# Kernel tuning notes

Hardware: AMD Instinct MI355X
Metric: run time of the kernel (lower is better)

Reference implementation:

```python
import jax, jax.numpy as jnp
import numpy as np

N_NODES = 100000
N_EDGES = 1600000
IN_CH, HID_CH, OUT_CH = 128, 128, 64


def setup_inputs() -> dict:
    key = jax.random.key(0)
    ks = jax.random.split(key, 9)
    x = jax.random.normal(ks[0], (N_NODES, IN_CH), dtype=jnp.float32)
    edge_index = jax.random.randint(ks[1], (2, N_EDGES), 0, N_NODES, dtype=jnp.int64)
    def glorot(k, shape):
        fan_in = shape[1]
        return jax.random.normal(k, shape, dtype=jnp.float32) / jnp.sqrt(jnp.float32(fan_in))
    return {
        "x": x,
        "edge_index": edge_index,
        "W1_l": glorot(ks[2], (HID_CH, IN_CH)),
        "W1_r": glorot(ks[3], (HID_CH, IN_CH)),
        "b1": jnp.zeros((HID_CH,), jnp.float32),
        "W2_l": glorot(ks[4], (HID_CH, HID_CH)),
        "W2_r": glorot(ks[5], (HID_CH, HID_CH)),
        "b2": jnp.zeros((HID_CH,), jnp.float32),
        "W3_l": glorot(ks[6], (OUT_CH, HID_CH)),
        "W3_r": glorot(ks[7], (OUT_CH, HID_CH)),
        "b3": jnp.zeros((OUT_CH,), jnp.float32),
    }


def _sage_conv(x, src, dst, W_l, W_r, b):
    # PyG SAGEConv (aggr='mean', root_weight=True): out = lin_l(mean_j x_j) + lin_r(x_i)
    n = x.shape[0]
    msg = x[src]                                            # [E, C] gather at source
    agg = jax.ops.segment_sum(msg, dst, num_segments=n)     # [N, C] scatter-sum at dest
    cnt = jax.ops.segment_sum(jnp.ones((src.shape[0],), x.dtype), dst, num_segments=n)
    mean = agg / jnp.maximum(cnt, 1.0)[:, None]             # zero-in-degree nodes -> 0
    return mean @ W_l.T + x @ W_r.T + b


def reference(x, edge_index, W1_l, W1_r, b1, W2_l, W2_r, b2, W3_l, W3_r, b3):
    src, dst = edge_index[0], edge_index[1]
    h = jax.nn.relu(_sage_conv(x, src, dst, W1_l, W1_r, b1))
    # F.dropout with training=False is identity (eval mode)
    h = jax.nn.relu(_sage_conv(h, src, dst, W2_l, W2_r, b2))
    return _sage_conv(h, src, dst, W3_l, W3_r, b3)
```

## Files before the change

### kernel.cpp

```cpp
#include <hip/hip_runtime.h>
#include <hip/hip_bf16.h>
#include <cstddef>
#include <cstdint>

#define NBLK(n, b) (((n) + (b) - 1) / (b))

typedef __attribute__((ext_vector_type(8))) short short8;
typedef __attribute__((ext_vector_type(4))) float f32x4;

__device__ inline unsigned short f2bf(float f) {
  union { float f; unsigned u; } v; v.f = f;
  unsigned u = v.u;
  u += 0x7FFFu + ((u >> 16) & 1u);
  return (unsigned short)(u >> 16);
}
__device__ inline float bflo(unsigned u) { union { unsigned u; float f; } v; v.u = u << 16; return v.f; }
__device__ inline float bfhi(unsigned u) { union { unsigned u; float f; } v; v.u = u & 0xFFFF0000u; return v.f; }


__global__ void k_detect(const unsigned* __restrict__ edges, int* __restrict__ flag) {
  if (threadIdx.x == 0 && blockIdx.x == 0) {
    int is64 = 1;
#pragma unroll
    for (int i = 0; i < 16; ++i)
      if (edges[2 * i + 1] != 0u) is64 = 0;
    *flag = is64;
  }
}

__global__ void k_zero_int(int* __restrict__ p, int n) {
  int i = blockIdx.x * blockDim.x + threadIdx.x;
  if (i < n) p[i] = 0;
}

__global__ void k_cast(const float* __restrict__ x, unsigned* __restrict__ xb, int total2) {
  int i = blockIdx.x * blockDim.x + threadIdx.x;
  if (i >= total2) return;
  float2 v = *(const float2*)(x + (size_t)i * 2);
  xb[i] = (unsigned)f2bf(v.x) | ((unsigned)f2bf(v.y) << 16);
}

__global__ void k_prep_w(const float* __restrict__ Wl, const float* __restrict__ Wr,
                         unsigned short* __restrict__ Wb, int total) {
  int i = blockIdx.x * blockDim.x + threadIdx.x;
  if (i >= total) return;
  int nrow = i >> 8, k = i & 255;
  float v = (k < 128) ? Wr[nrow * 128 + k] : Wl[nrow * 128 + (k - 128)];
  Wb[i] = f2bf(v);
}

__global__ void k_hist_rank(const void* __restrict__ edges, const int* __restrict__ flag,
                            int* __restrict__ deg, int* __restrict__ rank, int E) {
  int e = blockIdx.x * blockDim.x + threadIdx.x;
  if (e >= E) return;
  int d;
  if (*flag) d = (int)((const long long*)edges)[(size_t)E + e];
  else       d = ((const int*)edges)[(size_t)E + e];
  rank[e] = atomicAdd(&deg[d], 1);
}

__global__ void k_scan1(const int* __restrict__ deg, int* __restrict__ rowptr,
                        int* __restrict__ partials, int n) {
  __shared__ int sd[256];
  int t = threadIdx.x;
  int base = blockIdx.x * 1024 + t * 4;
  int v[4];
  int sum = 0;
#pragma unroll
  for (int i = 0; i < 4; ++i) {
    int idx = base + i;
    v[i] = (idx < n) ? deg[idx] : 0;
    sum += v[i];
  }
  sd[t] = sum;
  __syncthreads();
  for (int off = 1; off < 256; off <<= 1) {
    int xv = (t >= off) ? sd[t - off] : 0;
    __syncthreads();
    sd[t] += xv;
    __syncthreads();
  }
  int run = sd[t] - sum;
#pragma unroll
  for (int i = 0; i < 4; ++i) {
    int idx = base + i;
    if (idx < n) rowptr[idx] = run;
    run += v[i];
  }
  if (t == 0) partials[blockIdx.x] = sd[255];
}

__global__ void k_scan2(int* __restrict__ partials, int nb) {
  __shared__ int sd[256];
  int t = threadIdx.x;
  int v = (t < nb) ? partials[t] : 0;
  sd[t] = v;
  __syncthreads();
  for (int off = 1; off < 256; off <<= 1) {
    int xv = (t >= off) ? sd[t - off] : 0;
    __syncthreads();
    sd[t] += xv;
    __syncthreads();
  }
  if (t < nb) partials[t] = sd[t] - v;
}

__global__ void k_scan_add(int* __restrict__ rowptr, const int* __restrict__ partials, int n, int E) {
  int i = blockIdx.x * blockDim.x + threadIdx.x;
  if (i < n) rowptr[i] += partials[i >> 10];
  if (blockIdx.x == 0 && threadIdx.x == 0) rowptr[n] = E;
}

__global__ void k_fill2(const void* __restrict__ edges, const int* __restrict__ flag,
                        const int* __restrict__ rowptr, const int* __restrict__ rank,
                        int* __restrict__ srcSorted, int E) {
  int e = blockIdx.x * blockDim.x + threadIdx.x;
  if (e >= E) return;
  int s, d;
  if (*flag) {
    const long long* p = (const long long*)edges;
    s = (int)p[e];
    d = (int)p[(size_t)E + e];
  } else {
    const int* p = (const int*)edges;
    s = p[e];
    d = p[(size_t)E + e];
  }
  srcSorted[rowptr[d] + rank[e]] = s;
}

__global__ void k_aggregate(const unsigned* __restrict__ in, const int* __restrict__ rowptr,
                            const int* __restrict__ srcs, unsigned* __restrict__ mean, int n) {
  int lane = threadIdx.x & 63;
  int w = threadIdx.x >> 6;
  int node = blockIdx.x * 4 + w;
  if (node >= n) return;
  int r0 = rowptr[node], r1 = rowptr[node + 1];
  int sub = lane & 15;
  int eg = lane >> 4;
  float acc[8];
#pragma unroll
  for (int k = 0; k < 8; ++k) acc[k] = 0.f;

  for (int base = r0; base < r1; base += 64) {
    int e = base + lane;
    int sv = (e < r1) ? srcs[e] : 0;
    int cnt = min(64, r1 - base);
    int j = 0;
    for (; j + 8 <= cnt; j += 8) {
      int s0 = __shfl(sv, j + eg);
      int s1 = __shfl(sv, j + 4 + eg);
      uint4 u0 = *(const uint4*)(in + (size_t)s0 * 64 + sub * 4);
      uint4 u1 = *(const uint4*)(in + (size_t)s1 * 64 + sub * 4);
      acc[0] += bflo(u0.x); acc[1] += bfhi(u0.x);
      acc[2] += bflo(u0.y); acc[3] += bfhi(u0.y);
      acc[4] += bflo(u0.z); acc[5] += bfhi(u0.z);
      acc[6] += bflo(u0.w); acc[7] += bfhi(u0.w);
      acc[0] += bflo(u1.x); acc[1] += bfhi(u1.x);
      acc[2] += bflo(u1.y); acc[3] += bfhi(u1.y);
      acc[4] += bflo(u1.z); acc[5] += bfhi(u1.z);
      acc[6] += bflo(u1.w); acc[7] += bfhi(u1.w);
    }
    for (; j < cnt; j += 4) {
      int jj = j + eg;
      int s = __shfl(sv, jj);
      if (jj < cnt) {
        uint4 u = *(const uint4*)(in + (size_t)s * 64 + sub * 4);
        acc[0] += bflo(u.x); acc[1] += bfhi(u.x);
        acc[2] += bflo(u.y); acc[3] += bfhi(u.y);
        acc[4] += bflo(u.z); acc[5] += bfhi(u.z);
        acc[6] += bflo(u.w); acc[7] += bfhi(u.w);
      }
    }
  }

#pragma unroll
  for (int k = 0; k < 8; ++k) {
    acc[k] += __shfl_down(acc[k], 32);
    acc[k] += __shfl_down(acc[k], 16);
  }
  if (eg == 0) {
    float sc = 1.0f / (float)max(r1 - r0, 1);
    uint4 o;
    o.x = (unsigned)f2bf(acc[0] * sc) | ((unsigned)f2bf(acc[1] * sc) << 16);
    o.y = (unsigned)f2bf(acc[2] * sc) | ((unsigned)f2bf(acc[3] * sc) << 16);
    o.z = (unsigned)f2bf(acc[4] * sc) | ((unsigned)f2bf(acc[5] * sc) << 16);
    o.w = (unsigned)f2bf(acc[6] * sc) | ((unsigned)f2bf(acc[7] * sc) << 16);
    *(uint4*)(mean + (size_t)node * 64 + sub * 4) = o;
  }
}

template <int H, bool RELU, bool BF16OUT>
__global__ __launch_bounds__(256) void k_gemm(
    const unsigned short* __restrict__ selfB, const unsigned short* __restrict__ meanB,
    const unsigned short* __restrict__ Wb, const float* __restrict__ bias,
    void* __restrict__ outp, int n) {
  constexpr int TN = H / 32;
  int lane = threadIdx.x & 63;
  int w = threadIdx.x >> 6;
  int wr = w & 1, wc = w >> 1;
  int nodeBase = blockIdx.x * 128 + wr * 64;
  int colBase = wc * (H / 2);
  int l15 = lane & 15, quad = lane >> 4;

  f32x4 acc[4][TN];
#pragma unroll
  for (int t = 0; t < 4; ++t)
#pragma unroll
    for (int j = 0; j < TN; ++j) acc[t][j] = (f32x4){0.f, 0.f, 0.f, 0.f};

#pragma unroll
  for (int c = 0; c < 8; ++c) {
    const unsigned short* A = (c < 4) ? selfB : meanB;
    int ko = (c & 3) * 32 + quad * 8;
    short8 af[4], bfr[TN];
#pragma unroll
    for (int t = 0; t < 4; ++t) {
      int row = nodeBase + t * 16 + l15;
      row = min(row, n - 1);
      af[t] = *(const short8*)(A + (size_t)row * 128 + ko);
    }
#pragma unroll
    for (int j = 0; j < TN; ++j) {
      int cn = colBase + j * 16 + l15;
      bfr[j] = *(const short8*)(Wb + (size_t)cn * 256 + c * 32 + quad * 8);
    }
#pragma unroll
    for (int t = 0; t < 4; ++t)
#pragma unroll
      for (int j = 0; j < TN; ++j)
        acc[t][j] = __builtin_amdgcn_mfma_f32_16x16x32_bf16(af[t], bfr[j], acc[t][j], 0, 0, 0);
  }

#pragma unroll
  for (int j = 0; j < TN; ++j) {
    int col = colBase + j * 16 + l15;
    float bv = bias[col];
#pragma unroll
    for (int t = 0; t < 4; ++t) {
#pragma unroll
      for (int r = 0; r < 4; ++r) {
        int row = nodeBase + t * 16 + quad * 4 + r;
        if (row < n) {
          float v = acc[t][j][r] + bv;
          if (RELU) v = fmaxf(v, 0.f);
          if (BF16OUT) ((unsigned short*)outp)[(size_t)row * H + col] = f2bf(v);
          else ((float*)outp)[(size_t)row * H + col] = v;
        }
      }
    }
  }
}


extern "C" void kernel_launch(void* const* d_in, const int* in_sizes, int n_in,
                              void* d_out, int out_size, void* d_ws, size_t ws_size,
                              hipStream_t stream) {
  (void)n_in; (void)out_size; (void)ws_size;
  const float* x = (const float*)d_in[0];
  const void* edges = d_in[1];
  const float* W1l = (const float*)d_in[2];
  const float* W1r = (const float*)d_in[3];
  const float* b1 = (const float*)d_in[4];
  const float* W2l = (const float*)d_in[5];
  const float* W2r = (const float*)d_in[6];
  const float* b2 = (const float*)d_in[7];
  const float* W3l = (const float*)d_in[8];
  const float* W3r = (const float*)d_in[9];
  const float* b3 = (const float*)d_in[10];
  float* out = (float*)d_out;

  const int N = in_sizes[0] / 128;
  const int E = in_sizes[1] / 2;

  char* ws = (char*)d_ws;
  size_t off = 0;
  auto alloc = [&](size_t bytes) -> char* {
    char* p = ws + off;
    off = (off + bytes + 255) & ~(size_t)255;
    return p;
  };
  int* flag = (int*)alloc(4);
  int* deg = (int*)alloc((size_t)N * 4);
  int* rowptr = (int*)alloc((size_t)(N + 1) * 4);
  int* rank = (int*)alloc((size_t)E * 4);
  int* partials = (int*)alloc(4096);
  int* srcSorted = (int*)alloc((size_t)E * 4);
  unsigned short* xb = (unsigned short*)alloc((size_t)N * 128 * 2);
  unsigned short* mean = (unsigned short*)alloc((size_t)N * 128 * 2);
  unsigned short* h1 = (unsigned short*)alloc((size_t)N * 128 * 2);
  unsigned short* h2 = (unsigned short*)alloc((size_t)N * 128 * 2);
  unsigned short* Wb1 = (unsigned short*)alloc(128 * 256 * 2);
  unsigned short* Wb2 = (unsigned short*)alloc(128 * 256 * 2);
  unsigned short* Wb3 = (unsigned short*)alloc(64 * 256 * 2);

  int nb1 = (N + 1023) / 1024;

  k_detect<<<1, 64, 0, stream>>>((const unsigned*)edges, flag);
  k_zero_int<<<NBLK(N, 256), 256, 0, stream>>>(deg, N);
  k_cast<<<NBLK(N * 64, 256), 256, 0, stream>>>(x, (unsigned*)xb, N * 64);
  k_prep_w<<<NBLK(128 * 256, 256), 256, 0, stream>>>(W1l, W1r, Wb1, 128 * 256);
  k_prep_w<<<NBLK(128 * 256, 256), 256, 0, stream>>>(W2l, W2r, Wb2, 128 * 256);
  k_prep_w<<<NBLK(64 * 256, 256), 256, 0, stream>>>(W3l, W3r, Wb3, 64 * 256);
  k_hist_rank<<<NBLK(E, 256), 256, 0, stream>>>(edges, flag, deg, rank, E);
  k_scan1<<<nb1, 256, 0, stream>>>(deg, rowptr, partials, N);
  k_scan2<<<1, 256, 0, stream>>>(partials, nb1);
  k_scan_add<<<NBLK(N, 256), 256, 0, stream>>>(rowptr, partials, N, E);
  k_fill2<<<NBLK(E, 256), 256, 0, stream>>>(edges, flag, rowptr, rank, srcSorted, E);

  int gAgg = NBLK(N, 4);
  int gGemm = NBLK(N, 128);

  k_aggregate<<<gAgg, 256, 0, stream>>>((const unsigned*)xb, rowptr, srcSorted, (unsigned*)mean, N);
  k_gemm<128, true, true><<<gGemm, 256, 0, stream>>>(xb, mean, Wb1, b1, h1, N);
  k_aggregate<<<gAgg, 256, 0, stream>>>((const unsigned*)h1, rowptr, srcSorted, (unsigned*)mean, N);
  k_gemm<128, true, true><<<gGemm, 256, 0, stream>>>(h1, mean, Wb2, b2, h2, N);
  k_aggregate<<<gAgg, 256, 0, stream>>>((const unsigned*)h2, rowptr, srcSorted, (unsigned*)mean, N);
  k_gemm<64, false, false><<<gGemm, 256, 0, stream>>>(h2, mean, Wb3, b3, out, N);
}
```

Baseline: 522.5 us.

## Replace global-atomic CSR build with two-level bucketed counting sort

Builds the CSR through a bucketed counting sort instead of a per-edge global atomic histogram and scattered fill. Edges are first bucketed by destination block of 512 nodes using shared-memory histograms. Each bucket is then sorted locally in shared memory to produce rowptr and srcSorted. The cast, weight prep, zeroing and format detection kernels are merged into one setup launch to cut launch count. This removes heavily contended global atomics and random scatters, but packs the source and local destination into 32 bits, which assumes node ids below 2^17.

```diff
diff --git a/kernel.cpp b/kernel.cpp
--- a/kernel.cpp
+++ b/kernel.cpp
@@ -17,59 +17,89 @@
 __device__ inline float bflo(unsigned u) { union { unsigned u; float f; } v; v.u = u << 16; return v.f; }
 __device__ inline float bfhi(unsigned u) { union { unsigned u; float f; } v; v.u = u & 0xFFFF0000u; return v.f; }
 
-
-__global__ void k_detect(const unsigned* __restrict__ edges, int* __restrict__ flag) {
-  if (threadIdx.x == 0 && blockIdx.x == 0) {
-    int is64 = 1;
-#pragma unroll
-    for (int i = 0; i < 16; ++i)
-      if (edges[2 * i + 1] != 0u) is64 = 0;
-    *flag = is64;
-  }
-}
-
-__global__ void k_zero_int(int* __restrict__ p, int n) {
-  int i = blockIdx.x * blockDim.x + threadIdx.x;
-  if (i < n) p[i] = 0;
-}
-
-__global__ void k_cast(const float* __restrict__ x, unsigned* __restrict__ xb, int total2) {
-  int i = blockIdx.x * blockDim.x + threadIdx.x;
-  if (i >= total2) return;
-  float2 v = *(const float2*)(x + (size_t)i * 2);
-  xb[i] = (unsigned)f2bf(v.x) | ((unsigned)f2bf(v.y) << 16);
-}
-
-__global__ void k_prep_w(const float* __restrict__ Wl, const float* __restrict__ Wr,
-                         unsigned short* __restrict__ Wb, int total) {
-  int i = blockIdx.x * blockDim.x + threadIdx.x;
-  if (i >= total) return;
+#define BSHIFT 9
+#define BSIZE 512
+
+
+__device__ inline void prep_w_dev(const float* __restrict__ Wl, const float* __restrict__ Wr,
+                                  unsigned short* __restrict__ Wb, int b) {
+  int i = b * 256 + threadIdx.x;
   int nrow = i >> 8, k = i & 255;
   float v = (k < 128) ? Wr[nrow * 128 + k] : Wl[nrow * 128 + (k - 128)];
   Wb[i] = f2bf(v);
 }
 
-__global__ void k_hist_rank(const void* __restrict__ edges, const int* __restrict__ flag,
-                            int* __restrict__ deg, int* __restrict__ rank, int E) {
-  int e = blockIdx.x * blockDim.x + threadIdx.x;
-  if (e >= E) return;
-  int d;
-  if (*flag) d = (int)((const long long*)edges)[(size_t)E + e];
-  else       d = ((const int*)edges)[(size_t)E + e];
-  rank[e] = atomicAdd(&deg[d], 1);
-}
-
-__global__ void k_scan1(const int* __restrict__ deg, int* __restrict__ rowptr,
-                        int* __restrict__ partials, int n) {
+__global__ void k_setup(const float* __restrict__ x, unsigned* __restrict__ xb, int N,
+                        int* __restrict__ bucketCnt, int NB,
+                        const float* __restrict__ W1l, const float* __restrict__ W1r, unsigned short* __restrict__ Wb1,
+                        const float* __restrict__ W2l, const float* __restrict__ W2r, unsigned short* __restrict__ Wb2,
+                        const float* __restrict__ W3l, const float* __restrict__ W3r, unsigned short* __restrict__ Wb3,
+                        const unsigned* __restrict__ edges, int* __restrict__ flag) {
+  int b = blockIdx.x;
+  int gCast = (N * 64 + 255) >> 8;
+  if (b < gCast) {
+    int i = b * 256 + threadIdx.x;
+    if (i < N * 64) {
+      float2 v = *(const float2*)(x + (size_t)i * 2);
+      xb[i] = (unsigned)f2bf(v.x) | ((unsigned)f2bf(v.y) << 16);
+    }
+    return;
+  }
+  b -= gCast;
+  if (b < 128) { prep_w_dev(W1l, W1r, Wb1, b); return; }
+  b -= 128;
+  if (b < 128) { prep_w_dev(W2l, W2r, Wb2, b); return; }
+  b -= 128;
+  if (b < 64) { prep_w_dev(W3l, W3r, Wb3, b); return; }
+  b -= 64;
+  if (b == 0) {
+    for (int i = threadIdx.x; i < NB; i += 256) bucketCnt[i] = 0;
+    if (threadIdx.x == 0) {
+      int is64 = 1;
+#pragma unroll
+      for (int i = 0; i < 16; ++i)
+        if (edges[2 * i + 1] != 0u) is64 = 0;
+      *flag = is64;
+    }
+  }
+}
+
+
+__global__ __launch_bounds__(256) void k_bhist(const void* __restrict__ edges, const int* __restrict__ flag,
+                                               int* __restrict__ bucketCnt, int E, int NB) {
+  __shared__ int h[1024];
+  for (int i = threadIdx.x; i < NB; i += 256) h[i] = 0;
+  __syncthreads();
+  int base_e = blockIdx.x * 4096;
+  bool is64 = (*flag) != 0;
+#pragma unroll
+  for (int k = 0; k < 16; ++k) {
+    int e = base_e + k * 256 + threadIdx.x;
+    if (e < E) {
+      int d;
+      if (is64) d = (int)((const long long*)edges)[(size_t)E + e];
+      else      d = ((const int*)edges)[(size_t)E + e];
+      atomicAdd(&h[d >> BSHIFT], 1);
+    }
+  }
+  __syncthreads();
+  for (int i = threadIdx.x; i < NB; i += 256) {
+    int c = h[i];
+    if (c) atomicAdd(&bucketCnt[i], c);
+  }
+}
+
+__global__ void k_bscan(const int* __restrict__ bucketCnt, int* __restrict__ bucketBase,
+                        int* __restrict__ bucketCursor, int NB, int E) {
   __shared__ int sd[256];
   int t = threadIdx.x;
-  int base = blockIdx.x * 1024 + t * 4;
+  int base = t * 4;
   int v[4];
   int sum = 0;
 #pragma unroll
   for (int i = 0; i < 4; ++i) {
     int idx = base + i;
-    v[i] = (idx < n) ? deg[idx] : 0;
+    v[i] = (idx < NB) ? bucketCnt[idx] : 0;
     sum += v[i];
   }
   sd[t] = sum;
@@ -84,17 +114,80 @@
 #pragma unroll
   for (int i = 0; i < 4; ++i) {
     int idx = base + i;
-    if (idx < n) rowptr[idx] = run;
+    if (idx < NB) { bucketBase[idx] = run; bucketCursor[idx] = run; }
     run += v[i];
   }
-  if (t == 0) partials[blockIdx.x] = sd[255];
-}
-
-__global__ void k_scan2(int* __restrict__ partials, int nb) {
+  if (t == 0) bucketBase[NB] = E;
+}
+
+__global__ __launch_bounds__(256) void k_bscatter(const void* __restrict__ edges, const int* __restrict__ flag,
+                                                  int* __restrict__ bucketCursor, unsigned* __restrict__ bucketed,
+                                                  int E, int NB) {
+  __shared__ int h[1024];
+  __shared__ int base[1024];
+  for (int i = threadIdx.x; i < NB; i += 256) h[i] = 0;
+  __syncthreads();
+  int base_e = blockIdx.x * 4096;
+  bool is64 = (*flag) != 0;
+  unsigned key[16];
+  int bkt[16];
+#pragma unroll
+  for (int k = 0; k < 16; ++k) {
+    int e = base_e + k * 256 + threadIdx.x;
+    bkt[k] = -1;
+    if (e < E) {
+      int s, d;
+      if (is64) {
+        s = (int)((const long long*)edges)[e];
+        d = (int)((const long long*)edges)[(size_t)E + e];
+      } else {
+        s = ((const int*)edges)[e];
+        d = ((const int*)edges)[(size_t)E + e];
+      }
+      bkt[k] = d >> BSHIFT;
+      key[k] = (unsigned)s | ((unsigned)(d & (BSIZE - 1)) << 17);
+      atomicAdd(&h[bkt[k]], 1);
+    }
+  }
+  __syncthreads();
+  for (int i = threadIdx.x; i < NB; i += 256) {
+    int c = h[i];
+    base[i] = c ? atomicAdd(&bucketCursor[i], c) : 0;
+    h[i] = 0;
+  }
+  __syncthreads();
+#pragma unroll
+  for (int k = 0; k < 16; ++k) {
+    if (bkt[k] >= 0) {
+      int r = atomicAdd(&h[bkt[k]], 1);
+      bucketed[base[bkt[k]] + r] = key[k];
+    }
+  }
+}
+
+__global__ __launch_bounds__(256) void k_csr(const unsigned* __restrict__ bucketed,
+                                             const int* __restrict__ bucketBase,
+                                             int* __restrict__ rowptr, int* __restrict__ srcSorted,
+                                             int N, int E, int NB) {
+  __shared__ int h[512];
+  __shared__ int excl[512];
   __shared__ int sd[256];
+  int b = blockIdx.x;
   int t = threadIdx.x;
-  int v = (t < nb) ? partials[t] : 0;
-  sd[t] = v;
+  int nodeBase = b << BSHIFT;
+  int nNode = min(BSIZE, N - nodeBase);
+  int s0 = bucketBase[b], s1 = bucketBase[b + 1];
+  int cnt = s1 - s0;
+  h[t * 2] = 0; h[t * 2 + 1] = 0;
+  __syncthreads();
+  for (int i = t; i < cnt; i += 256) {
+    int ld = bucketed[s0 + i] >> 17;
+    atomicAdd(&h[ld], 1);
+  }
+  __syncthreads();
+  int a0 = h[t * 2], a1 = h[t * 2 + 1];
+  int s = a0 + a1;
+  sd[t] = s;
   __syncthreads();
   for (int off = 1; off < 256; off <<= 1) {
     int xv = (t >= off) ? sd[t - off] : 0;
@@ -102,31 +195,20 @@
     sd[t] += xv;
     __syncthreads();
   }
-  if (t < nb) partials[t] = sd[t] - v;
-}
-
-__global__ void k_scan_add(int* __restrict__ rowptr, const int* __restrict__ partials, int n, int E) {
-  int i = blockIdx.x * blockDim.x + threadIdx.x;
-  if (i < n) rowptr[i] += partials[i >> 10];
-  if (blockIdx.x == 0 && threadIdx.x == 0) rowptr[n] = E;
-}
-
-__global__ void k_fill2(const void* __restrict__ edges, const int* __restrict__ flag,
-                        const int* __restrict__ rowptr, const int* __restrict__ rank,
-                        int* __restrict__ srcSorted, int E) {
-  int e = blockIdx.x * blockDim.x + threadIdx.x;
-  if (e >= E) return;
-  int s, d;
-  if (*flag) {
-    const long long* p = (const long long*)edges;
-    s = (int)p[e];
-    d = (int)p[(size_t)E + e];
-  } else {
-    const int* p = (const int*)edges;
-    s = p[e];
-    d = p[(size_t)E + e];
-  }
-  srcSorted[rowptr[d] + rank[e]] = s;
+  int run = sd[t] - s;
+  excl[t * 2] = run;
+  excl[t * 2 + 1] = run + a0;
+  if (t * 2 < nNode) rowptr[nodeBase + t * 2] = s0 + run;
+  if (t * 2 + 1 < nNode) rowptr[nodeBase + t * 2 + 1] = s0 + run + a0;
+  if (b == NB - 1 && t == 0) rowptr[N] = E;
+  h[t * 2] = 0; h[t * 2 + 1] = 0;
+  __syncthreads();
+  for (int i = t; i < cnt; i += 256) {
+    unsigned u = bucketed[s0 + i];
+    int ld = u >> 17;
+    int r = atomicAdd(&h[ld], 1);
+    srcSorted[s0 + excl[ld] + r] = (int)(u & 0x1FFFFu);
+  }
 }
 
 __global__ void k_aggregate(const unsigned* __restrict__ in, const int* __restrict__ rowptr,
@@ -272,6 +354,7 @@
 
   const int N = in_sizes[0] / 128;
   const int E = in_sizes[1] / 2;
+  const int NB = (N + BSIZE - 1) >> BSHIFT;
 
   char* ws = (char*)d_ws;
   size_t off = 0;
@@ -281,10 +364,11 @@
     return p;
   };
   int* flag = (int*)alloc(4);
-  int* deg = (int*)alloc((size_t)N * 4);
+  int* bucketCnt = (int*)alloc((size_t)NB * 4);
+  int* bucketBase = (int*)alloc((size_t)(NB + 1) * 4);
+  int* bucketCursor = (int*)alloc((size_t)NB * 4);
+  unsigned* bucketed = (unsigned*)alloc((size_t)E * 4);
   int* rowptr = (int*)alloc((size_t)(N + 1) * 4);
-  int* rank = (int*)alloc((size_t)E * 4);
-  int* partials = (int*)alloc(4096);
   int* srcSorted = (int*)alloc((size_t)E * 4);
   unsigned short* xb = (unsigned short*)alloc((size_t)N * 128 * 2);
   unsigned short* mean = (unsigned short*)alloc((size_t)N * 128 * 2);
@@ -294,19 +378,16 @@
   unsigned short* Wb2 = (unsigned short*)alloc(128 * 256 * 2);
   unsigned short* Wb3 = (unsigned short*)alloc(64 * 256 * 2);
 
-  int nb1 = (N + 1023) / 1024;
-
-  k_detect<<<1, 64, 0, stream>>>((const unsigned*)edges, flag);
-  k_zero_int<<<NBLK(N, 256), 256, 0, stream>>>(deg, N);
-  k_cast<<<NBLK(N * 64, 256), 256, 0, stream>>>(x, (unsigned*)xb, N * 64);
-  k_prep_w<<<NBLK(128 * 256, 256), 256, 0, stream>>>(W1l, W1r, Wb1, 128 * 256);
-  k_prep_w<<<NBLK(128 * 256, 256), 256, 0, stream>>>(W2l, W2r, Wb2, 128 * 256);
-  k_prep_w<<<NBLK(64 * 256, 256), 256, 0, stream>>>(W3l, W3r, Wb3, 64 * 256);
-  k_hist_rank<<<NBLK(E, 256), 256, 0, stream>>>(edges, flag, deg, rank, E);
-  k_scan1<<<nb1, 256, 0, stream>>>(deg, rowptr, partials, N);
-  k_scan2<<<1, 256, 0, stream>>>(partials, nb1);
-  k_scan_add<<<NBLK(N, 256), 256, 0, stream>>>(rowptr, partials, N, E);
-  k_fill2<<<NBLK(E, 256), 256, 0, stream>>>(edges, flag, rowptr, rank, srcSorted, E);
+  int gSetup = NBLK(N * 64, 256) + 128 + 128 + 64 + 1;
+  int gE = NBLK(E, 4096);
+
+  k_setup<<<gSetup, 256, 0, stream>>>(x, (unsigned*)xb, N, bucketCnt, NB,
+                                      W1l, W1r, Wb1, W2l, W2r, Wb2, W3l, W3r, Wb3,
+                                      (const unsigned*)edges, flag);
+  k_bhist<<<gE, 256, 0, stream>>>(edges, flag, bucketCnt, E, NB);
+  k_bscan<<<1, 256, 0, stream>>>(bucketCnt, bucketBase, bucketCursor, NB, E);
+  k_bscatter<<<gE, 256, 0, stream>>>(edges, flag, bucketCursor, bucketed, E, NB);
+  k_csr<<<NB, 256, 0, stream>>>(bucketed, bucketBase, rowptr, srcSorted, N, E, NB);
 
   int gAgg = NBLK(N, 4);
   int gGemm = NBLK(N, 128);
```

New measurement: 472.5 us. 1.11x faster.
